# Optimization experiments

Hardware: AMD Instinct MI355X
Metric: run time of the kernel (lower is better)

## Reference

```python
import jax, jax.numpy as jnp
import numpy as np

B, L, V, E, H, T, TD, R, RE = 16, 128, 32000, 256, 256, 10, 32, 24, 128


def _gru_dir(x, h0, w_ih, w_hh, b_ih, b_hh, reverse):
    # x: [B,L,Din], h0: [B,H]; PyTorch GRU gate math (r,z,n ordering)
    if reverse:
        x = jnp.flip(x, 1)
    gi = jnp.einsum('bld,gd->blg', x, w_ih) + b_ih  # [B,L,3H] input gates precomputed

    def step(h, gi_t):
        gh = h @ w_hh.T + b_hh
        ir, iz, inn = jnp.split(gi_t, 3, -1)
        hr, hz, hn = jnp.split(gh, 3, -1)
        r = jax.nn.sigmoid(ir + hr)
        z = jax.nn.sigmoid(iz + hz)
        n = jnp.tanh(inn + r * hn)
        hnew = (1.0 - z) * n + z * h
        return hnew, hnew

    hT, ys = jax.lax.scan(step, h0, jnp.swapaxes(gi, 0, 1))
    ys = jnp.swapaxes(ys, 0, 1)  # [B,L,H]
    if reverse:
        ys = jnp.flip(ys, 1)
    return ys, hT


def _bigru_layer(x, h0f, h0b, w_ih, w_hh, b_ih, b_hh):
    yf, hf = _gru_dir(x, h0f, w_ih[0], w_hh[0], b_ih[0], b_hh[0], False)
    yb, hb = _gru_dir(x, h0b, w_ih[1], w_hh[1], b_ih[1], b_hh[1], True)
    return jnp.concatenate([yf, yb], -1), hf, hb


def _crf_llh(em, tags, mask, start, trans, end):
    # torchcrf log-likelihood, batch_first, reduction='sum'. em: [B,L,T]
    score = start[tags[:, 0]] + jnp.take_along_axis(em[:, 0], tags[:, 0:1], -1)[:, 0]
    em_t = jnp.swapaxes(em, 0, 1)
    tg_t = jnp.swapaxes(tags, 0, 1)
    mk_t = jnp.swapaxes(mask, 0, 1)

    def num_step(s, inp):
        e, tp, tc, m = inp
        s = s + (trans[tp, tc] + jnp.take_along_axis(e, tc[:, None], -1)[:, 0]) * m
        return s, None

    score, _ = jax.lax.scan(num_step, score, (em_t[1:], tg_t[:-1], tg_t[1:], mk_t[1:]))
    seq_ends = jnp.sum(mask, 1).astype(jnp.int32) - 1
    last = jnp.take_along_axis(tags, seq_ends[:, None], 1)[:, 0]
    score = score + end[last]

    alpha = start[None] + em[:, 0]  # [B,T]

    def den_step(a, inp):
        e, m = inp
        nxt = jax.nn.logsumexp(a[:, :, None] + trans[None] + e[:, None, :], axis=1)
        return jnp.where(m[:, None] > 0, nxt, a), None

    alpha, _ = jax.lax.scan(den_step, alpha, (em_t[1:], mk_t[1:]))
    logZ = jax.nn.logsumexp(alpha + end[None], axis=1)
    return jnp.sum(score - logZ)


def _joint_forward(text, tags, gold_rel, mask, h0, emb_word, emb_tok, emb_rel,
                   wih0, whh0, bih0, bhh0, wih1, whh1, bih1, bhh1,
                   whp, bhp, wlp, blp, wner, bner, cs, ct, ce,
                   wu, bu, wv, bv, wuv, buv):
    x = emb_word[text]  # [B,L,E]
    y0, hf0, hb0 = _bigru_layer(x, h0[0], h0[1], wih0, whh0, bih0, bhh0)
    out, hf1, hb1 = _bigru_layer(y0, h0[2], h0[3], wih1, whh1, bih1, bhh1)  # [B,L,2H]
    h_n = jnp.stack([hf0, hb0, hf1, hb1], 0)  # [4,B,H]

    # attention network
    out_sq = out @ whp.T + bhp  # [B,L,H]
    hsq = (jnp.transpose(h_n, (1, 2, 0)) @ wlp.T + blp)[:, :, 0]  # [B,H]
    attw = jax.nn.softmax(jnp.einsum('bh,blh->bl', hsq, out_sq), -1)[:, :, None]  # [B,L,1]

    ner_in = jnp.concatenate([out, attw], -1)  # [B,L,2H+1]
    ner_score = ner_in @ wner.T + bner  # [B,L,T]
    loss_ner = -_crf_llh(ner_score, tags, mask, cs, ct, ce)

    # teacher-forcing branch: labels == token_type_list
    rel_in = jnp.concatenate([out, emb_tok[tags], attw], -1)  # [B,L,2H+TD+1]
    U = rel_in @ wu.T + bu   # [B,L,RE]  (u: unsqueeze(1) -> varies over j)
    Vp = rel_in @ wv.T + bv  # [B,L,RE]  (v: unsqueeze(2) -> varies over i)
    # selection_uv(cat(u,v)) is linear -> exact additive decomposition avoids the [B,L,L,2RE] concat
    A = U @ wuv[:, :RE].T            # contribution of u (index j)
    C = Vp @ wuv[:, RE:].T + buv     # contribution of v (index i)
    uv = jnp.tanh(A[:, None, :, :] + C[:, :, None, :])  # [B,L,L,RE]
    # einsum('bijh,rh->birj') followed by permute(0,1,3,2) == 'bijh,rh->bijr'
    logits = jnp.einsum('bijh,rh->bijr', uv, emb_rel)  # [B,L,L,R]

    pair_mask = (mask[:, :, None] * mask[:, None, :])[..., None]  # [B,L,L,1]
    gold_oh = jax.nn.one_hot(gold_rel, R, dtype=logits.dtype)
    wrel = jnp.full((R,), 50.0, logits.dtype).at[0].set(1.0)
    pwrel = jnp.full((R,), 20.0, logits.dtype).at[0].set(1.0)
    bce = -wrel * (pwrel * gold_oh * jax.nn.log_sigmoid(logits)
                   + (1.0 - gold_oh) * jax.nn.log_sigmoid(-logits))
    loss_rel = jnp.sum(bce * pair_mask) / jnp.sum(mask)
    return loss_ner, loss_rel


def setup_inputs():
    key = jax.random.key(0)
    ks = jax.random.split(key, 40)

    def nrm(i, shape, s=0.05):
        return jax.random.normal(ks[i], shape, jnp.float32) * s

    return {
        'text_tokened': jax.random.randint(ks[0], (B, L), 0, V, jnp.int32),
        'token_type_list': jax.random.randint(ks[1], (B, L), 0, T, jnp.int32),
        'pred_rel_matrix': jax.random.randint(ks[2], (B, L, L), 0, R, jnp.int32),
        'mask_tokens': jnp.ones((B, L), jnp.float32),
        'hidden_init': nrm(3, (4, B, H), 1.0),
        'emb_word': nrm(4, (V, E)),
        'emb_tok': nrm(5, (T, TD)),
        'emb_rel': nrm(6, (R, RE)),
        'gru_w_ih_l0': nrm(7, (2, 3 * H, E)),
        'gru_w_hh_l0': nrm(8, (2, 3 * H, H)),
        'gru_b_ih_l0': nrm(9, (2, 3 * H)),
        'gru_b_hh_l0': nrm(10, (2, 3 * H)),
        'gru_w_ih_l1': nrm(11, (2, 3 * H, 2 * H)),
        'gru_w_hh_l1': nrm(12, (2, 3 * H, H)),
        'gru_b_ih_l1': nrm(13, (2, 3 * H)),
        'gru_b_hh_l1': nrm(14, (2, 3 * H)),
        'w_hp': nrm(15, (H, 2 * H)),
        'b_hp': nrm(16, (H,)),
        'w_lp': nrm(17, (1, 4)),
        'b_lp': nrm(18, (1,)),
        'w_ner': nrm(19, (T, 2 * H + 1)),
        'b_ner': nrm(20, (T,)),
        'crf_start': nrm(21, (T,)),
        'crf_trans': nrm(22, (T, T)),
        'crf_end': nrm(23, (T,)),
        'w_u': nrm(24, (RE, 2 * H + TD + 1)),
        'b_u': nrm(25, (RE,)),
        'w_v': nrm(26, (RE, 2 * H + TD + 1)),
        'b_v': nrm(27, (RE,)),
        'w_uv': nrm(28, (RE, 2 * RE)),
        'b_uv': nrm(29, (RE,)),
    }


def reference(text_tokened, token_type_list, pred_rel_matrix, mask_tokens, hidden_init,
              emb_word, emb_tok, emb_rel, gru_w_ih_l0, gru_w_hh_l0, gru_b_ih_l0, gru_b_hh_l0,
              gru_w_ih_l1, gru_w_hh_l1, gru_b_ih_l1, gru_b_hh_l1, w_hp, b_hp, w_lp, b_lp,
              w_ner, b_ner, crf_start, crf_trans, crf_end, w_u, b_u, w_v, b_v, w_uv, b_uv):
    return _joint_forward(text_tokened, token_type_list, pred_rel_matrix, mask_tokens, hidden_init,
                          emb_word, emb_tok, emb_rel, gru_w_ih_l0, gru_w_hh_l0, gru_b_ih_l0, gru_b_hh_l0,
                          gru_w_ih_l1, gru_w_hh_l1, gru_b_ih_l1, gru_b_hh_l1, w_hp, b_hp, w_lp, b_lp,
                          w_ner, b_ner, crf_start, crf_trans, crf_end, w_u, b_u, w_v, b_v, w_uv, b_uv)
```

## Files before the change

kernel.cpp:

```cpp
#include <hip/hip_runtime.h>

typedef unsigned short u16;
typedef unsigned char u8;
typedef unsigned long long u64;
typedef __attribute__((ext_vector_type(4))) float f32x4;
typedef __attribute__((ext_vector_type(8))) short bf16x8;

#define BL 2048

__device__ __forceinline__ u16 f2bf(float f) {
  unsigned u = __float_as_uint(f);
  u += 0x7fffu + ((u >> 16) & 1u);
  return (u16)(u >> 16);
}
__device__ __forceinline__ float bf2f(u16 x) {
  return __uint_as_float(((unsigned)x) << 16);
}
__device__ __forceinline__ u8 f2e4m3(float f) {
  unsigned u = __float_as_uint(f);
  unsigned s = (u >> 24) & 0x80u;
  float a = fabsf(f);
  a = fminf(a, 448.f);
  if (a < 0.015625f) {
    int m = (int)(a * 512.f + 0.5f);
    return (u8)(s | (unsigned)m);
  }
  unsigned au = __float_as_uint(a);
  au += 0x7ffffu + ((au >> 20) & 1u);
  unsigned e = (au >> 23) - 127u + 7u;
  unsigned m = (au >> 20) & 7u;
  return (u8)(s | (e << 3) | m);
}
__device__ __forceinline__ float sigm(float x) {
  float e = __expf(-fabsf(x));
  float s = 1.f / (1.f + e);
  return x >= 0.f ? s : 1.f - s;
}
__device__ __forceinline__ float tanh_s(float x) {
  float e = __expf(-2.f * fabsf(x));
  float t = (1.f - e) / (1.f + e);
  return x >= 0.f ? t : -t;
}

__global__ void prep_kernel(const float* __restrict__ wih0, const float* __restrict__ wih1,
                            const float* __restrict__ whp, const float* __restrict__ wu,
                            const float* __restrict__ wv, const float* __restrict__ wuv,
                            const float* __restrict__ bu, const float* __restrict__ bv,
                            const float* __restrict__ whh0, const float* __restrict__ whh1,
                            const float* __restrict__ bih0, const float* __restrict__ bhh0,
                            const float* __restrict__ bih1, const float* __restrict__ bhh1,
                            u16* __restrict__ o_wih0, u16* __restrict__ o_wih1,
                            u16* __restrict__ o_whp, u16* __restrict__ o_wuvpad,
                            u16* __restrict__ o_wuvc, float* __restrict__ o_buv2,
                            float* __restrict__ scal, u8* __restrict__ o_wf8,
                            float* __restrict__ o_bc, float* __restrict__ o_bhhn) {
  long i = (long)blockIdx.x * 256 + threadIdx.x;
  const long c1 = 393216, c2 = 1179648, c3 = 1310720, c4 = 1458176,
             c5 = 1490944, c6 = 1491200, c7 = 1491216,
             c8 = 2277648, c9 = 2280720, c10 = 2281744;
  if (i < c1) { o_wih0[i] = f2bf(wih0[i]); return; }
  if (i < c2) { long j = i - c1; o_wih1[j] = f2bf(wih1[j]); return; }
  if (i < c3) { long j = i - c2; o_whp[j] = f2bf(whp[j]); return; }
  if (i < c4) {
    long j = i - c3; int n = (int)(j / 576), k = (int)(j % 576);
    float v = 0.f;
    if (k < 545) v = (n < 128) ? wu[n * 545 + k] : wv[(n - 128) * 545 + k];
    o_wuvpad[j] = f2bf(v); return;
  }
  if (i < c5) {
    long j = i - c4; int n = (int)(j / 128), k = (int)(j % 128);
    float v = (n < 128) ? wuv[n * 256 + k] : wuv[(n - 128) * 256 + 128 + k];
    o_wuvc[j] = f2bf(v); return;
  }
  if (i < c6) { int n = (int)(i - c5); o_buv2[n] = (n < 128) ? bu[n] : bv[n - 128]; return; }
  if (i < c7) { scal[i - c6] = 0.f; return; }
  if (i < c8) {
    long j = i - c7;
    int layer = (int)(j / 393216);
    long r = j % 393216;
    float v = layer ? whh1[r] : whh0[r];
    o_wf8[j] = f2e4m3(v); return;
  }
  if (i < c9) {
    long j = i - c8;
    int layer = (int)(j / 1536);
    int k2 = (int)(j % 1536);
    float v = (layer ? bih1[k2] : bih0[k2]);
    if ((k2 % 768) < 512) v += (layer ? bhh1[k2] : bhh0[k2]);
    o_bc[j] = v; return;
  }
  if (i < c10) {
    long j = i - c9;
    int layer = (int)(j / 512);
    int k3 = (int)(j % 512);
    int idx = (k3 / 256) * 768 + 512 + (k3 % 256);
    o_bhhn[j] = layer ? bhh1[idx] : bhh0[idx];
    return;
  }
}

__global__ void gather_x(const int* __restrict__ text, const float* __restrict__ embw,
                         u16* __restrict__ xbf) {
  int i = blockIdx.x * 256 + threadIdx.x;
  if (i >= BL * 256) return;
  int bl = i >> 8, k = i & 255;
  xbf[i] = f2bf(embw[(long)text[bl] * 256 + k]);
}

__global__ __launch_bounds__(256) void gemm_bf16(
    const u16* __restrict__ A, int lda, const u16* __restrict__ Bm,
    const float* __restrict__ bias, float* __restrict__ C, u16* __restrict__ Cbf,
    int ldc, int M, int N, int K, int gimode) {
  __shared__ u16 As[64 * 40];
  __shared__ u16 Bs[64 * 40];
  const int tid = threadIdx.x;
  const int w = tid >> 6, l = tid & 63, c = l & 15, q = l >> 4;
  const int m0 = blockIdx.x * 64, n0 = blockIdx.y * 64;
  const int srow = tid >> 2, sq = tid & 3;
  f32x4 zero = {0.f, 0.f, 0.f, 0.f};
  f32x4 acc[4] = {zero, zero, zero, zero};
  for (int k0 = 0; k0 < K; k0 += 32) {
    *(bf16x8*)(As + srow * 40 + sq * 8) =
        *(const bf16x8*)(A + (long)(m0 + srow) * lda + k0 + sq * 8);
    *(bf16x8*)(Bs + srow * 40 + sq * 8) =
        *(const bf16x8*)(Bm + (long)(n0 + srow) * K + k0 + sq * 8);
    __syncthreads();
    bf16x8 a = *(const bf16x8*)(As + (w * 16 + c) * 40 + q * 8);
#pragma unroll
    for (int nt = 0; nt < 4; ++nt) {
      bf16x8 b = *(const bf16x8*)(Bs + (nt * 16 + c) * 40 + q * 8);
      acc[nt] = __builtin_amdgcn_mfma_f32_16x16x32_bf16(a, b, acc[nt], 0, 0, 0);
    }
    __syncthreads();
  }
#pragma unroll
  for (int nt = 0; nt < 4; ++nt) {
    int n = n0 + nt * 16 + c;
    float bv = bias ? bias[n] : 0.f;
#pragma unroll
    for (int r = 0; r < 4; ++r) {
      int m = m0 + w * 16 + q * 4 + r;
      float v = acc[nt][r] + bv;
      long off;
      if (gimode) {
        int t = m & 127, b = m >> 7;
        int dir = (n >= 768) ? 1 : 0;
        int rest = n - dir * 768;
        int g = rest >> 8, d = rest & 255;
        off = ((((long)t * 2 + dir) * 4 + (b >> 2)) * 3 + g) * 1024 + (b & 3) * 256 + d;
      } else {
        off = (long)m * ldc + n;
      }
      if (C) C[off] = v;
      if (Cbf) Cbf[off] = f2bf(v);
    }
  }
}

__global__ __launch_bounds__(1024) void gru_scan(
    const u16* __restrict__ gi4,
    const u8* __restrict__ wf8l,
    const float* __restrict__ bhhn_l,
    const float* __restrict__ h0,
    int layer, float* __restrict__ hn,
    u16* __restrict__ ybf)
{
  __shared__ u8 hq[2][16 * 264];
  __shared__ float accs[3][4][264];
  const int dir = blockIdx.x, bg = blockIdx.y;
  const int tid = threadIdx.x;
  const int w = tid >> 6, l = tid & 63, c = l & 15, q = l >> 4;
  const int hd = w * 16 + c;
  const u8* wdir = wf8l + (long)dir * 768 * 256;

  long Breg[8][3];
#pragma unroll
  for (int kt = 0; kt < 8; ++kt)
#pragma unroll
    for (int g = 0; g < 3; ++g)
      Breg[kt][g] = *(const long*)(wdir + (long)(g * 256 + hd) * 256 + kt * 32 + q * 8);

  const float bias_n = bhhn_l[dir * 256 + hd];
  const int hbase = (layer * 2 + dir) * (16 * 256);

  for (int e = tid; e < 1056; e += 1024) ((u64*)hq)[e] = 0ull;
  __syncthreads();
  float hprev = h0[hbase + (bg * 4 + q) * 256 + hd];
  hq[0][q * 264 + hd] = f2e4m3(hprev);

  const int tt0 = dir ? 127 : 0;
  const long gstep = dir ? -24576 : 24576;
  const long ystep = dir ? -512 : 512;
  const u16* gp = gi4 + ((long)(tt0 * 2 + dir) * 4 + bg) * 3072 + q * 256 + hd;
  u16* yp = ybf + ((long)((bg * 4 + q) * 128) + tt0) * 512 + dir * 256 + hd;

  u16 gAr = gp[0], gAz = gp[1024], gAn = gp[2048];
  const u16* gp1 = gp + gstep;
  u16 gBr = gp1[0], gBz = gp1[1024], gBn = gp1[2048];
  const u16* gpp = gp + 2 * gstep;
  __syncthreads();

#pragma unroll 1
  for (int t = 0; t < 128; t += 2) {
    {
      f32x4 a0 = {0.f, 0.f, 0.f, 0.f}, a1 = a0, a2 = a0;
#pragma unroll
      for (int kt = 0; kt < 8; ++kt) {
        long a = *(const long*)(hq[0] + c * 264 + kt * 32 + q * 8);
        a0 = __builtin_amdgcn_mfma_f32_16x16x32_fp8_fp8(a, Breg[kt][0], a0, 0, 0, 0);
        a1 = __builtin_amdgcn_mfma_f32_16x16x32_fp8_fp8(a, Breg[kt][1], a1, 0, 0, 0);
        a2 = __builtin_amdgcn_mfma_f32_16x16x32_fp8_fp8(a, Breg[kt][2], a2, 0, 0, 0);
      }
      if (q == 0) {
#pragma unroll
        for (int r = 0; r < 4; ++r) {
          accs[0][r][hd] = a0[r];
          accs[1][r][hd] = a1[r];
          accs[2][r][hd] = a2[r];
        }
      }
      asm volatile("s_waitcnt lgkmcnt(0)" ::: "memory");
      float rg = sigm(bf2f(gAr) + accs[0][q][hd]);
      float zg = sigm(bf2f(gAz) + accs[1][q][hd]);
      float ng = tanh_s(bf2f(gAn) + rg * (accs[2][q][hd] + bias_n));
      float hv = (1.f - zg) * ng + zg * hprev;
      hprev = hv;
      yp[0] = f2bf(hv);
      hq[1][q * 264 + hd] =
          (u8)(__builtin_amdgcn_cvt_pk_fp8_f32(hv, hv, 0, false) & 0xff);
      if (t < 126) { gAr = gpp[0]; gAz = gpp[1024]; gAn = gpp[2048]; gpp += gstep; }
      yp += ystep;
      asm volatile("s_waitcnt lgkmcnt(0)\n\ts_barrier" ::: "memory");
    }
    {
      f32x4 a0 = {0.f, 0.f, 0.f, 0.f}, a1 = a0, a2 = a0;
#pragma unroll
      for (int kt = 0; kt < 8; ++kt) {
        long a = *(const long*)(hq[1] + c * 264 + kt * 32 + q * 8);
        a0 = __builtin_amdgcn_mfma_f32_16x16x32_fp8_fp8(a, Breg[kt][0], a0, 0, 0, 0);
        a1 = __builtin_amdgcn_mfma_f32_16x16x32_fp8_fp8(a, Breg[kt][1], a1, 0, 0, 0);
        a2 = __builtin_amdgcn_mfma_f32_16x16x32_fp8_fp8(a, Breg[kt][2], a2, 0, 0, 0);
      }
      if (q == 0) {
#pragma unroll
        for (int r = 0; r < 4; ++r) {
          accs[0][r][hd] = a0[r];
          accs[1][r][hd] = a1[r];
          accs[2][r][hd] = a2[r];
        }
      }
      asm volatile("s_waitcnt lgkmcnt(0)" ::: "memory");
      float rg = sigm(bf2f(gBr) + accs[0][q][hd]);
      float zg = sigm(bf2f(gBz) + accs[1][q][hd]);
      float ng = tanh_s(bf2f(gBn) + rg * (accs[2][q][hd] + bias_n));
      float hv = (1.f - zg) * ng + zg * hprev;
      hprev = hv;
      yp[0] = f2bf(hv);
      hq[0][q * 264 + hd] =
          (u8)(__builtin_amdgcn_cvt_pk_fp8_f32(hv, hv, 0, false) & 0xff);
      if (t < 125) { gBr = gpp[0]; gBz = gpp[1024]; gBn = gpp[2048]; gpp += gstep; }
      yp += ystep;
      asm volatile("s_waitcnt lgkmcnt(0)\n\ts_barrier" ::: "memory");
    }
  }
  hn[hbase + (bg * 4 + q) * 256 + hd] = hprev;
}

__global__ void attn_kernel(const float* __restrict__ hn, const float* __restrict__ wlp,
                            const float* __restrict__ blp, const float* __restrict__ outsq,
                            float* __restrict__ attw) {
  int b = blockIdx.x, tid = threadIdx.x;
  __shared__ float hsq[256];
  __shared__ float sc[128];
  __shared__ float red[2];
  {
    float s = blp[0];
#pragma unroll
    for (int d = 0; d < 4; ++d) s += hn[d * 4096 + b * 256 + tid] * wlp[d];
    hsq[tid] = s;
  }
  __syncthreads();
  if (tid < 128) {
    float s = 0.f;
    const float* op = outsq + (long)(b * 128 + tid) * 256;
    for (int h = 0; h < 256; ++h) s += hsq[h] * op[h];
    sc[tid] = s;
  }
  __syncthreads();
  if (tid == 0) {
    float m = sc[0];
    for (int i = 1; i < 128; ++i) m = fmaxf(m, sc[i]);
    red[0] = m;
  }
  __syncthreads();
  if (tid < 128) sc[tid] = __expf(sc[tid] - red[0]);
  __syncthreads();
  if (tid == 0) {
    float s = 0.f;
    for (int i = 0; i < 128; ++i) s += sc[i];
    red[1] = s;
  }
  __syncthreads();
  if (tid < 128) attw[b * 128 + tid] = sc[tid] / red[1];
}

__global__ void build_relin(const u16* __restrict__ outbf, const int* __restrict__ tags,
                            const float* __restrict__ emb_tok, const float* __restrict__ attw,
                            u16* __restrict__ relin) {
  int i = blockIdx.x * 256 + threadIdx.x;
  if (i >= BL * 576) return;
  int bl = i / 576, cc = i % 576;
  u16 v;
  if (cc < 512) v = outbf[(long)bl * 512 + cc];
  else if (cc < 544) v = f2bf(emb_tok[tags[bl] * 32 + (cc - 512)]);
  else if (cc == 544) v = f2bf(attw[bl]);
  else v = 0;
  relin[i] = v;
}

__global__ __launch_bounds__(256) void ner_kernel(
    const u16* __restrict__ outbf, const float* __restrict__ attw,
    const float* __restrict__ wner, const float* __restrict__ bner,
    float* __restrict__ ner) {
  __shared__ float wn[10 * 513];
  int tid = threadIdx.x;
  for (int e = tid; e < 5130; e += 256) wn[e] = wner[e];
  __syncthreads();
  int row0 = blockIdx.x * 64;
  for (int o = tid; o < 640; o += 256) {
    int rr = o / 10, t = o % 10;
    int row = row0 + rr;
    const u16* op = outbf + (long)row * 512;
    const float* wp = wn + t * 513;
    float s = bner[t] + attw[row] * wp[512];
    for (int k = 0; k < 512; ++k) s += bf2f(op[k]) * wp[k];
    ner[(long)row * 10 + t] = s;
  }
}

__global__ __launch_bounds__(512) void rel_kernel(
    const float* __restrict__ AC,
    const int* __restrict__ gold,
    const float* __restrict__ mask,
    const float* __restrict__ embr,
    float* __restrict__ acc_out) {
  __shared__ float Au[32 * 132];
  __shared__ float Cv[32 * 132];
  __shared__ float ER[24 * 128];
  __shared__ int GT[32 * 33];
  __shared__ float Mi[32], Mj[32];
  __shared__ float redbuf[8];
  int b = blockIdx.x, it = blockIdx.y, jt = blockIdx.z;
  int i0 = it * 32, j0 = jt * 32;
  int tid = threadIdx.x;
  for (int e = tid; e < 4096; e += 512) {
    int rr = e >> 7, h = e & 127;
    Au[rr * 132 + h] = AC[(long)(b * 128 + j0 + rr) * 256 + h];
    Cv[rr * 132 + h] = AC[(long)(b * 128 + i0 + rr) * 256 + 128 + h];
  }
  for (int e = tid; e < 3072; e += 512) ER[e] = embr[e];
  for (int e = tid; e < 1024; e += 512) {
    int ii = e >> 5, jj = e & 31;
    GT[ii * 33 + jj] = gold[(long)b * 16384 + (i0 + ii) * 128 + (j0 + jj)];
  }
  if (tid < 32) Mi[tid] = mask[b * 128 + i0 + tid];
  else if (tid < 64) Mj[tid - 32] = mask[b * 128 + j0 + tid - 32];
  __syncthreads();
  float sum = 0.f;
#pragma unroll 1
  for (int k = 0; k < 2; ++k) {
    int p = tid + k * 512;
    int ii = p >> 5, jj = p & 31;
    float pm = Mi[ii] * Mj[jj];
    int g = GT[ii * 33 + jj];
    float logits[24];
#pragma unroll
    for (int r = 0; r < 24; ++r) logits[r] = 0.f;
#pragma unroll 1
    for (int hc = 0; hc < 4; ++hc) {
      float tt[32];
#pragma unroll
      for (int x4 = 0; x4 < 8; ++x4) {
        float4 a4 = *(const float4*)(Au + jj * 132 + hc * 32 + x4 * 4);
        float4 c4 = *(const float4*)(Cv + ii * 132 + hc * 32 + x4 * 4);
        tt[x4 * 4 + 0] = tanh_s(a4.x + c4.x);
        tt[x4 * 4 + 1] = tanh_s(a4.y + c4.y);
        tt[x4 * 4 + 2] = tanh_s(a4.z + c4.z);
        tt[x4 * 4 + 3] = tanh_s(a4.w + c4.w);
      }
#pragma unroll
      for (int r = 0; r < 24; ++r) {
        float s = logits[r];
#pragma unroll
        for (int x4 = 0; x4 < 8; ++x4) {
          float4 e4 = *(const float4*)(ER + r * 128 + hc * 32 + x4 * 4);
          s += tt[x4 * 4] * e4.x + tt[x4 * 4 + 1] * e4.y +
               tt[x4 * 4 + 2] * e4.z + tt[x4 * 4 + 3] * e4.w;
        }
        logits[r] = s;
      }
    }
    float lsum = 0.f;
#pragma unroll
    for (int r = 0; r < 24; ++r) {
      float x = logits[r];
      float e = __expf(-fabsf(x));
      float l1p = __logf(1.f + e);
      float lsp = fminf(x, 0.f) - l1p;
      float lsn = fminf(-x, 0.f) - l1p;
      float wr = r ? 50.f : 1.f;
      float pw = r ? 20.f : 1.f;
      lsum -= (r == g) ? (wr * pw * lsp) : (wr * lsn);
    }
    sum += lsum * pm;
  }
  for (int off = 32; off > 0; off >>= 1) sum += __shfl_down(sum, off, 64);
  if ((tid & 63) == 0) redbuf[tid >> 6] = sum;
  __syncthreads();
  if (tid == 0) {
    float s = 0.f;
    for (int x = 0; x < 8; ++x) s += redbuf[x];
    atomicAdd(acc_out, s);
  }
}

__global__ __launch_bounds__(512) void crf_kernel(
    const float* __restrict__ ner, const int* __restrict__ tags,
    const float* __restrict__ mask, const float* __restrict__ cs,
    const float* __restrict__ ct, const float* __restrict__ ce,
    float* __restrict__ scal) {
  __shared__ float tr[100];
  __shared__ float alpha[2][16][12];
  __shared__ float logZ[16], sc[16];
  __shared__ float red[8];
  int tid = threadIdx.x;
  if (tid < 100) tr[tid] = ct[tid];
  __syncthreads();
  int b = tid / 10, j = tid % 10;
  if (tid < 160) alpha[0][b][j] = cs[j] + ner[(long)(b * 128) * 10 + j];
  __syncthreads();
  int cur = 0;
  for (int t = 1; t < 128; ++t) {
    if (tid < 160) {
      float m = -1e30f;
#pragma unroll
      for (int i = 0; i < 10; ++i) m = fmaxf(m, alpha[cur][b][i] + tr[i * 10 + j]);
      float s = 0.f;
#pragma unroll
      for (int i = 0; i < 10; ++i) s += __expf(alpha[cur][b][i] + tr[i * 10 + j] - m);
      float v = m + __logf(s) + ner[(long)(b * 128 + t) * 10 + j];
      float mk = mask[b * 128 + t];
      alpha[1 - cur][b][j] = (mk > 0.f) ? v : alpha[cur][b][j];
    }
    __syncthreads();
    cur ^= 1;
  }
  if (tid < 16) {
    int bb = tid;
    float m = -1e30f;
    for (int jj = 0; jj < 10; ++jj) m = fmaxf(m, alpha[cur][bb][jj] + ce[jj]);
    float s = 0.f;
    for (int jj = 0; jj < 10; ++jj) s += __expf(alpha[cur][bb][jj] + ce[jj] - m);
    logZ[bb] = m + __logf(s);
    int tprev = tags[bb * 128];
    float sco = cs[tprev] + ner[(long)(bb * 128) * 10 + tprev];
    float msum_b = mask[bb * 128];
    for (int t = 1; t < 128; ++t) {
      int tc = tags[bb * 128 + t];
      float mk = mask[bb * 128 + t];
      sco += (tr[tprev * 10 + tc] + ner[(long)(bb * 128 + t) * 10 + tc]) * mk;
      msum_b += mk;
      tprev = tc;
    }
    int send = (int)(msum_b)-1;
    int last = tags[bb * 128 + send];
    sco += ce[last];
    sc[bb] = sco - logZ[bb];
  }
  float ms = 0.f;
  for (int e = tid; e < 2048; e += 512) ms += mask[e];
  for (int off = 32; off > 0; off >>= 1) ms += __shfl_down(ms, off, 64);
  if ((tid & 63) == 0) red[tid >> 6] = ms;
  __syncthreads();
  if (tid == 0) {
    float s = 0.f;
    for (int x = 0; x < 8; ++x) s += red[x];
    scal[1] = s;
    float llh = 0.f;
    for (int bb = 0; bb < 16; ++bb) llh += sc[bb];
    scal[0] = llh;
  }
}

__global__ void finalize_kernel(const float* __restrict__ scal, float* __restrict__ out) {
  if (threadIdx.x == 0 && blockIdx.x == 0) {
    out[0] = -scal[0];
    out[1] = scal[2] / scal[1];
  }
}

extern "C" void kernel_launch(void* const* d_in, const int* in_sizes, int n_in,
                              void* d_out, int out_size, void* d_ws, size_t ws_size,
                              hipStream_t stream) {
  (void)in_sizes; (void)n_in; (void)out_size; (void)ws_size;
  const int*   text = (const int*)d_in[0];
  const int*   tags = (const int*)d_in[1];
  const int*   gold = (const int*)d_in[2];
  const float* mask = (const float*)d_in[3];
  const float* h0   = (const float*)d_in[4];
  const float* embw = (const float*)d_in[5];
  const float* embt = (const float*)d_in[6];
  const float* embr = (const float*)d_in[7];
  const float* wih0 = (const float*)d_in[8];
  const float* whh0 = (const float*)d_in[9];
  const float* bih0 = (const float*)d_in[10];
  const float* bhh0 = (const float*)d_in[11];
  const float* wih1 = (const float*)d_in[12];
  const float* whh1 = (const float*)d_in[13];
  const float* bih1 = (const float*)d_in[14];
  const float* bhh1 = (const float*)d_in[15];
  const float* whp  = (const float*)d_in[16];
  const float* bhp  = (const float*)d_in[17];
  const float* wlp  = (const float*)d_in[18];
  const float* blp  = (const float*)d_in[19];
  const float* wner = (const float*)d_in[20];
  const float* bner = (const float*)d_in[21];
  const float* cs   = (const float*)d_in[22];
  const float* ct   = (const float*)d_in[23];
  const float* ce   = (const float*)d_in[24];
  const float* wu   = (const float*)d_in[25];
  const float* bu   = (const float*)d_in[26];
  const float* wv   = (const float*)d_in[27];
  const float* bv   = (const float*)d_in[28];
  const float* wuv  = (const float*)d_in[29];
  const float* buv  = (const float*)d_in[30];

  char* ws = (char*)d_ws;
  u16*   gi     = (u16*)(ws + 0);
  u16*   xbf    = (u16*)(ws + 12582912);
  u16*   y0bf   = (u16*)(ws + 13631488);
  u8*    wf8    = (u8*)(ws + 15728640);
  float* bc     = (float*)(ws + 16515072);
  float* bhhn   = (float*)(ws + 16527360);
  u16*   outbf  = (u16*)(ws + 19922944);
  float* hn     = (float*)(ws + 22020096);
  float* outsq  = (float*)(ws + 22085632);
  float* attw   = (float*)(ws + 24182784);
  u16*   relin  = (u16*)(ws + 24190976);
  u16*   uvbf   = (u16*)(ws + 28647424);
  float* ac32   = (float*)(ws + 29696000);
  float* ner    = (float*)(ws + 31793152);
  u16*   wih0b  = (u16*)(ws + 31875072);
  u16*   wih1b  = (u16*)(ws + 32661504);
  u16*   whpb   = (u16*)(ws + 34234368);
  u16*   wuvp   = (u16*)(ws + 34496512);
  u16*   wuvc   = (u16*)(ws + 34791424);
  float* buv2   = (float*)(ws + 34856960);
  float* scal   = (float*)(ws + 34859008);

  prep_kernel<<<8913, 256, 0, stream>>>(wih0, wih1, whp, wu, wv, wuv, bu, bv,
                                        whh0, whh1, bih0, bhh0, bih1, bhh1,
                                        wih0b, wih1b, whpb, wuvp, wuvc, buv2, scal,
                                        wf8, bc, bhhn);
  gather_x<<<2048, 256, 0, stream>>>(text, embw, xbf);
  gemm_bf16<<<dim3(32, 24), 256, 0, stream>>>(xbf, 256, wih0b, bc, nullptr, gi, 1536, 2048, 1536, 256, 1);
  gru_scan<<<dim3(2, 4), 1024, 0, stream>>>(gi, wf8, bhhn, h0, 0, hn, y0bf);
  gemm_bf16<<<dim3(32, 24), 256, 0, stream>>>(y0bf, 512, wih1b, bc + 1536, nullptr, gi, 1536, 2048, 1536, 512, 1);
  gru_scan<<<dim3(2, 4), 1024, 0, stream>>>(gi, wf8 + 393216, bhhn + 512, h0, 1, hn, outbf);
  gemm_bf16<<<dim3(32, 4), 256, 0, stream>>>(outbf, 512, whpb, bhp, outsq, nullptr, 256, 2048, 256, 512, 0);
  attn_kernel<<<16, 256, 0, stream>>>(hn, wlp, blp, outsq, attw);
  build_relin<<<4608, 256, 0, stream>>>(outbf, tags, embt, attw, relin);
  ner_kernel<<<32, 256, 0, stream>>>(outbf, attw, wner, bner, ner);
  gemm_bf16<<<dim3(32, 4), 256, 0, stream>>>(relin, 576, wuvp, buv2, nullptr, uvbf, 256, 2048, 256, 576, 0);
  gemm_bf16<<<dim3(32, 2), 256, 0, stream>>>(uvbf, 256, wuvc, nullptr, ac32, nullptr, 256, 2048, 128, 128, 0);
  gemm_bf16<<<dim3(32, 2), 256, 0, stream>>>(uvbf + 128, 256, wuvc + 128 * 128, buv, ac32 + 128, nullptr, 256, 2048, 128, 128, 0);
  rel_kernel<<<dim3(16, 4, 4), 512, 0, stream>>>(ac32, gold, mask, embr, scal + 2);
  crf_kernel<<<1, 512, 0, stream>>>(ner, tags, mask, cs, ct, ce, scal);
  finalize_kernel<<<1, 64, 0, stream>>>(scal, (float*)d_out);
}
```

Baseline: 750.9 us.

## Run GRU scan with one block per direction over all batches and fold small kernels

The GRU recurrence now runs in one 1024-thread block per direction that handles all 16 batch rows, instead of four blocks per direction each owning four rows. Each lane uses all four MFMA accumulator rows directly, which removes the shared-memory accumulator staging and its extra wait. The gate-input layout is changed so each lane loads four batch values with one 64-bit load. The embedding gather is folded into the prep kernel and the finalize kernel into the CRF kernel, cutting two launches. In exchange, each block does four times the pointwise gate math per step and the scan runs on fewer compute units.

```diff
diff --git a/kernel.cpp b/kernel.cpp
--- a/kernel.cpp
+++ b/kernel.cpp
@@ -49,15 +49,17 @@
                             const float* __restrict__ whh0, const float* __restrict__ whh1,
                             const float* __restrict__ bih0, const float* __restrict__ bhh0,
                             const float* __restrict__ bih1, const float* __restrict__ bhh1,
+                            const int* __restrict__ text, const float* __restrict__ embw,
                             u16* __restrict__ o_wih0, u16* __restrict__ o_wih1,
                             u16* __restrict__ o_whp, u16* __restrict__ o_wuvpad,
                             u16* __restrict__ o_wuvc, float* __restrict__ o_buv2,
                             float* __restrict__ scal, u8* __restrict__ o_wf8,
-                            float* __restrict__ o_bc, float* __restrict__ o_bhhn) {
+                            float* __restrict__ o_bc, float* __restrict__ o_bhhn,
+                            u16* __restrict__ o_xbf) {
   long i = (long)blockIdx.x * 256 + threadIdx.x;
   const long c1 = 393216, c2 = 1179648, c3 = 1310720, c4 = 1458176,
              c5 = 1490944, c6 = 1491200, c7 = 1491216,
-             c8 = 2277648, c9 = 2280720, c10 = 2281744;
+             c8 = 2277648, c9 = 2280720, c10 = 2281744, c11 = 2806032;
   if (i < c1) { o_wih0[i] = f2bf(wih0[i]); return; }
   if (i < c2) { long j = i - c1; o_wih1[j] = f2bf(wih1[j]); return; }
   if (i < c3) { long j = i - c2; o_whp[j] = f2bf(whp[j]); return; }
@@ -97,14 +99,12 @@
     o_bhhn[j] = layer ? bhh1[idx] : bhh0[idx];
     return;
   }
-}
-
-__global__ void gather_x(const int* __restrict__ text, const float* __restrict__ embw,
-                         u16* __restrict__ xbf) {
-  int i = blockIdx.x * 256 + threadIdx.x;
-  if (i >= BL * 256) return;
-  int bl = i >> 8, k = i & 255;
-  xbf[i] = f2bf(embw[(long)text[bl] * 256 + k]);
+  if (i < c11) {
+    long j = i - c10;
+    int bl = (int)(j >> 8), k = (int)(j & 255);
+    o_xbf[j] = f2bf(embw[(long)text[bl] * 256 + k]);
+    return;
+  }
 }
 
 __global__ __launch_bounds__(256) void gemm_bf16(
@@ -146,8 +146,7 @@
         int t = m & 127, b = m >> 7;
         int dir = (n >= 768) ? 1 : 0;
         int rest = n - dir * 768;
-        int g = rest >> 8, d = rest & 255;
-        off = ((((long)t * 2 + dir) * 4 + (b >> 2)) * 3 + g) * 1024 + (b & 3) * 256 + d;
+        off = ((long)(t * 2 + dir) * 768 + rest) * 16 + b;
       } else {
         off = (long)m * ldc + n;
       }
@@ -158,7 +157,7 @@
 }
 
 __global__ __launch_bounds__(1024) void gru_scan(
-    const u16* __restrict__ gi4,
+    const u16* __restrict__ gi2,
     const u8* __restrict__ wf8l,
     const float* __restrict__ bhhn_l,
     const float* __restrict__ h0,
@@ -166,8 +165,7 @@
     u16* __restrict__ ybf)
 {
   __shared__ u8 hq[2][16 * 264];
-  __shared__ float accs[3][4][264];
-  const int dir = blockIdx.x, bg = blockIdx.y;
+  const int dir = blockIdx.x;
   const int tid = threadIdx.x;
   const int w = tid >> 6, l = tid & 63, c = l & 15, q = l >> 4;
   const int hd = w * 16 + c;
@@ -183,20 +181,28 @@
   const float bias_n = bhhn_l[dir * 256 + hd];
   const int hbase = (layer * 2 + dir) * (16 * 256);
 
-  for (int e = tid; e < 1056; e += 1024) ((u64*)hq)[e] = 0ull;
-  __syncthreads();
-  float hprev = h0[hbase + (bg * 4 + q) * 256 + hd];
-  hq[0][q * 264 + hd] = f2e4m3(hprev);
+  float hprev[4];
+#pragma unroll
+  for (int r = 0; r < 4; ++r) {
+    int m = q * 4 + r;
+    hprev[r] = h0[hbase + m * 256 + hd];
+    hq[0][m * 264 + hd] = f2e4m3(hprev[r]);
+  }
 
   const int tt0 = dir ? 127 : 0;
   const long gstep = dir ? -24576 : 24576;
   const long ystep = dir ? -512 : 512;
-  const u16* gp = gi4 + ((long)(tt0 * 2 + dir) * 4 + bg) * 3072 + q * 256 + hd;
-  u16* yp = ybf + ((long)((bg * 4 + q) * 128) + tt0) * 512 + dir * 256 + hd;
-
-  u16 gAr = gp[0], gAz = gp[1024], gAn = gp[2048];
+  const int lo = hd * 16 + q * 4;
+  const u16* gp = gi2 + (long)(tt0 * 2 + dir) * 12288;
+  u16* yp = ybf + ((long)(q * 4) * 128 + tt0) * 512 + dir * 256 + hd;
+
+  u64 cgA0 = *(const u64*)(gp + lo);
+  u64 cgA1 = *(const u64*)(gp + lo + 4096);
+  u64 cgA2 = *(const u64*)(gp + lo + 8192);
   const u16* gp1 = gp + gstep;
-  u16 gBr = gp1[0], gBz = gp1[1024], gBn = gp1[2048];
+  u64 cgB0 = *(const u64*)(gp1 + lo);
+  u64 cgB1 = *(const u64*)(gp1 + lo + 4096);
+  u64 cgB2 = *(const u64*)(gp1 + lo + 8192);
   const u16* gpp = gp + 2 * gstep;
   __syncthreads();
 
@@ -211,24 +217,29 @@
         a1 = __builtin_amdgcn_mfma_f32_16x16x32_fp8_fp8(a, Breg[kt][1], a1, 0, 0, 0);
         a2 = __builtin_amdgcn_mfma_f32_16x16x32_fp8_fp8(a, Breg[kt][2], a2, 0, 0, 0);
       }
-      if (q == 0) {
-#pragma unroll
-        for (int r = 0; r < 4; ++r) {
-          accs[0][r][hd] = a0[r];
-          accs[1][r][hd] = a1[r];
-          accs[2][r][hd] = a2[r];
-        }
-      }
-      asm volatile("s_waitcnt lgkmcnt(0)" ::: "memory");
-      float rg = sigm(bf2f(gAr) + accs[0][q][hd]);
-      float zg = sigm(bf2f(gAz) + accs[1][q][hd]);
-      float ng = tanh_s(bf2f(gAn) + rg * (accs[2][q][hd] + bias_n));
-      float hv = (1.f - zg) * ng + zg * hprev;
-      hprev = hv;
-      yp[0] = f2bf(hv);
-      hq[1][q * 264 + hd] =
-          (u8)(__builtin_amdgcn_cvt_pk_fp8_f32(hv, hv, 0, false) & 0xff);
-      if (t < 126) { gAr = gpp[0]; gAz = gpp[1024]; gAn = gpp[2048]; gpp += gstep; }
+      float hv4[4];
+#pragma unroll
+      for (int r = 0; r < 4; ++r) {
+        float rg = sigm(bf2f((u16)(cgA0 >> (16 * r))) + a0[r]);
+        float zg = sigm(bf2f((u16)(cgA1 >> (16 * r))) + a1[r]);
+        float ng = tanh_s(bf2f((u16)(cgA2 >> (16 * r))) + rg * (a2[r] + bias_n));
+        float hv = (1.f - zg) * ng + zg * hprev[r];
+        hprev[r] = hv;
+        hv4[r] = hv;
+        yp[r * 65536] = f2bf(hv);
+      }
+      int pk01 = __builtin_amdgcn_cvt_pk_fp8_f32(hv4[0], hv4[1], 0, false);
+      int pk23 = __builtin_amdgcn_cvt_pk_fp8_f32(hv4[2], hv4[3], 0, false);
+      hq[1][(q * 4 + 0) * 264 + hd] = (u8)(pk01 & 0xff);
+      hq[1][(q * 4 + 1) * 264 + hd] = (u8)((pk01 >> 8) & 0xff);
+      hq[1][(q * 4 + 2) * 264 + hd] = (u8)(pk23 & 0xff);
+      hq[1][(q * 4 + 3) * 264 + hd] = (u8)((pk23 >> 8) & 0xff);
+      if (t < 126) {
+        cgA0 = *(const u64*)(gpp + lo);
+        cgA1 = *(const u64*)(gpp + lo + 4096);
+        cgA2 = *(const u64*)(gpp + lo + 8192);
+        gpp += gstep;
+      }
       yp += ystep;
       asm volatile("s_waitcnt lgkmcnt(0)\n\ts_barrier" ::: "memory");
     }
@@ -241,29 +252,36 @@
         a1 = __builtin_amdgcn_mfma_f32_16x16x32_fp8_fp8(a, Breg[kt][1], a1, 0, 0, 0);
         a2 = __builtin_amdgcn_mfma_f32_16x16x32_fp8_fp8(a, Breg[kt][2], a2, 0, 0, 0);
       }
-      if (q == 0) {
-#pragma unroll
-        for (int r = 0; r < 4; ++r) {
-          accs[0][r][hd] = a0[r];
-          accs[1][r][hd] = a1[r];
-          accs[2][r][hd] = a2[r];
-        }
-      }
-      asm volatile("s_waitcnt lgkmcnt(0)" ::: "memory");
-      float rg = sigm(bf2f(gBr) + accs[0][q][hd]);
-      float zg = sigm(bf2f(gBz) + accs[1][q][hd]);
-      float ng = tanh_s(bf2f(gBn) + rg * (accs[2][q][hd] + bias_n));
-      float hv = (1.f - zg) * ng + zg * hprev;
-      hprev = hv;
-      yp[0] = f2bf(hv);
-      hq[0][q * 264 + hd] =
-          (u8)(__builtin_amdgcn_cvt_pk_fp8_f32(hv, hv, 0, false) & 0xff);
-      if (t < 125) { gBr = gpp[0]; gBz = gpp[1024]; gBn = gpp[2048]; gpp += gstep; }
+      float hv4[4];
+#pragma unroll
+      for (int r = 0; r < 4; ++r) {
+        float rg = sigm(bf2f((u16)(cgB0 >> (16 * r))) + a0[r]);
+        float zg = sigm(bf2f((u16)(cgB1 >> (16 * r))) + a1[r]);
+        float ng = tanh_s(bf2f((u16)(cgB2 >> (16 * r))) + rg * (a2[r] + bias_n));
+        float hv = (1.f - zg) * ng + zg * hprev[r];
+        hprev[r] = hv;
+        hv4[r] = hv;
+        yp[r * 65536] = f2bf(hv);
+      }
+      int pk01 = __builtin_amdgcn_cvt_pk_fp8_f32(hv4[0], hv4[1], 0, false);
+      int pk23 = __builtin_amdgcn_cvt_pk_fp8_f32(hv4[2], hv4[3], 0, false);
+      hq[0][(q * 4 + 0) * 264 + hd] = (u8)(pk01 & 0xff);
+      hq[0][(q * 4 + 1) * 264 + hd] = (u8)((pk01 >> 8) & 0xff);
+      hq[0][(q * 4 + 2) * 264 + hd] = (u8)(pk23 & 0xff);
+      hq[0][(q * 4 + 3) * 264 + hd] = (u8)((pk23 >> 8) & 0xff);
+      if (t < 125) {
+        cgB0 = *(const u64*)(gpp + lo);
+        cgB1 = *(const u64*)(gpp + lo + 4096);
+        cgB2 = *(const u64*)(gpp + lo + 8192);
+        gpp += gstep;
+      }
       yp += ystep;
       asm volatile("s_waitcnt lgkmcnt(0)\n\ts_barrier" ::: "memory");
     }
   }
-  hn[hbase + (bg * 4 + q) * 256 + hd] = hprev;
+#pragma unroll
+  for (int r = 0; r < 4; ++r)
+    hn[hbase + (q * 4 + r) * 256 + hd] = hprev[r];
 }
 
 __global__ void attn_kernel(const float* __restrict__ hn, const float* __restrict__ wlp,
@@ -428,7 +446,7 @@
     const float* __restrict__ ner, const int* __restrict__ tags,
     const float* __restrict__ mask, const float* __restrict__ cs,
     const float* __restrict__ ct, const float* __restrict__ ce,
-    float* __restrict__ scal) {
+    const float* __restrict__ scal, float* __restrict__ out) {
   __shared__ float tr[100];
   __shared__ float alpha[2][16][12];
   __shared__ float logZ[16], sc[16];
@@ -485,17 +503,10 @@
   if (tid == 0) {
     float s = 0.f;
     for (int x = 0; x < 8; ++x) s += red[x];
-    scal[1] = s;
     float llh = 0.f;
     for (int bb = 0; bb < 16; ++bb) llh += sc[bb];
-    scal[0] = llh;
-  }
-}
-
-__global__ void finalize_kernel(const float* __restrict__ scal, float* __restrict__ out) {
-  if (threadIdx.x == 0 && blockIdx.x == 0) {
-    out[0] = -scal[0];
-    out[1] = scal[2] / scal[1];
+    out[0] = -llh;
+    out[1] = scal[2] / s;
   }
 }
 
@@ -558,15 +569,15 @@
   float* buv2   = (float*)(ws + 34856960);
   float* scal   = (float*)(ws + 34859008);
 
-  prep_kernel<<<8913, 256, 0, stream>>>(wih0, wih1, whp, wu, wv, wuv, bu, bv,
-                                        whh0, whh1, bih0, bhh0, bih1, bhh1,
-                                        wih0b, wih1b, whpb, wuvp, wuvc, buv2, scal,
-                                        wf8, bc, bhhn);
-  gather_x<<<2048, 256, 0, stream>>>(text, embw, xbf);
+  prep_kernel<<<10962, 256, 0, stream>>>(wih0, wih1, whp, wu, wv, wuv, bu, bv,
+                                         whh0, whh1, bih0, bhh0, bih1, bhh1,
+                                         text, embw,
+                                         wih0b, wih1b, whpb, wuvp, wuvc, buv2, scal,
+                                         wf8, bc, bhhn, xbf);
   gemm_bf16<<<dim3(32, 24), 256, 0, stream>>>(xbf, 256, wih0b, bc, nullptr, gi, 1536, 2048, 1536, 256, 1);
-  gru_scan<<<dim3(2, 4), 1024, 0, stream>>>(gi, wf8, bhhn, h0, 0, hn, y0bf);
+  gru_scan<<<2, 1024, 0, stream>>>(gi, wf8, bhhn, h0, 0, hn, y0bf);
   gemm_bf16<<<dim3(32, 24), 256, 0, stream>>>(y0bf, 512, wih1b, bc + 1536, nullptr, gi, 1536, 2048, 1536, 512, 1);
-  gru_scan<<<dim3(2, 4), 1024, 0, stream>>>(gi, wf8 + 393216, bhhn + 512, h0, 1, hn, outbf);
+  gru_scan<<<2, 1024, 0, stream>>>(gi, wf8 + 393216, bhhn + 512, h0, 1, hn, outbf);
   gemm_bf16<<<dim3(32, 4), 256, 0, stream>>>(outbf, 512, whpb, bhp, outsq, nullptr, 256, 2048, 256, 512, 0);
   attn_kernel<<<16, 256, 0, stream>>>(hn, wlp, blp, outsq, attw);
   build_relin<<<4608, 256, 0, stream>>>(outbf, tags, embt, attw, relin);
@@ -575,6 +586,5 @@
   gemm_bf16<<<dim3(32, 2), 256, 0, stream>>>(uvbf, 256, wuvc, nullptr, ac32, nullptr, 256, 2048, 128, 128, 0);
   gemm_bf16<<<dim3(32, 2), 256, 0, stream>>>(uvbf + 128, 256, wuvc + 128 * 128, buv, ac32 + 128, nullptr, 256, 2048, 128, 128, 0);
   rel_kernel<<<dim3(16, 4, 4), 512, 0, stream>>>(ac32, gold, mask, embr, scal + 2);
-  crf_kernel<<<1, 512, 0, stream>>>(ner, tags, mask, cs, ct, ce, scal);
-  finalize_kernel<<<1, 64, 0, stream>>>(scal, (float*)d_out);
-}
+  crf_kernel<<<1, 512, 0, stream>>>(ner, tags, mask, cs, ct, ce, scal, (float*)d_out);
+}
```

Result: slower. 1.016 ms (+35.3%).
